# Performance work log

Measured on AMD Instinct MI355X. Metric: run time of the kernel, lower is better.

## Reference

```python
import jax, jax.numpy as jnp
import numpy as np

MASK_THRESHOLD = 0.5
NO_OVERLAP = True


def setup_inputs() -> dict:
    key = jax.random.key(0)
    B, N, C, M = 2, 50, 80, 28
    H, W = 800, 1333
    k1, k2, k3, k4, k5, k6, k7 = jax.random.split(key, 7)
    mask_outs = jax.random.uniform(k1, (B, N, C, M, M), dtype=jnp.float32)
    # valid xyxy boxes inside the image, 20-220 px per side
    cx = jax.random.uniform(k2, (B, N), dtype=jnp.float32) * W
    cy = jax.random.uniform(k3, (B, N), dtype=jnp.float32) * H
    bw = jax.random.uniform(k4, (B, N), dtype=jnp.float32) * 200.0 + 20.0
    bh = jax.random.uniform(k5, (B, N), dtype=jnp.float32) * 200.0 + 20.0
    boxes = jnp.stack([cx - bw / 2, cy - bh / 2, cx + bw / 2, cy + bh / 2], axis=-1)
    scores = jax.random.uniform(k6, (B, N), dtype=jnp.float32)
    class_ids = jax.random.randint(k7, (B, N), 0, C).astype(jnp.int64)
    return {"mask_outs": mask_outs, "boxes": boxes, "scores": scores,
            "class_ids": class_ids, "orig_h": H, "orig_w": W}


def _gather_rows(m, idx, size):
    # m: [Mh, Mw], idx: [L] int32 -> [L, Mw], zero outside [0, size)
    valid = (idx >= 0) & (idx < size)
    v = m[jnp.clip(idx, 0, size - 1)]
    return v * valid[:, None].astype(m.dtype)


def _gather_cols(m, idx, size):
    # m: [H, Mw], idx: [L] int32 -> [H, L], zero outside [0, size)
    valid = (idx >= 0) & (idx < size)
    v = m[:, jnp.clip(idx, 0, size - 1)]
    return v * valid[None, :].astype(m.dtype)


def _paste_soft(masks, boxes, H, W):
    # Equivalent to torch grid_sample(align_corners=False, zeros padding) on the
    # affine grid built from boxes (detectron2 _do_paste_mask), exploiting the
    # separable (outer-product) structure of the grid.
    # masks: [N, Mh, Mw], boxes: [N, 4] -> [N, H, W] float
    N, Mh, Mw = masks.shape
    x0, y0, x1, y1 = (boxes[:, 0:1], boxes[:, 1:2], boxes[:, 2:3], boxes[:, 3:4])
    img_y = jnp.arange(H, dtype=masks.dtype) + 0.5  # [H]
    img_x = jnp.arange(W, dtype=masks.dtype) + 0.5  # [W]
    gy = (img_y[None, :] - y0) / (y1 - y0) * 2.0 - 1.0  # [N, H] normalized
    gx = (img_x[None, :] - x0) / (x1 - x0) * 2.0 - 1.0  # [N, W]
    iy = ((gy + 1.0) * Mh - 1.0) / 2.0  # unnormalize, align_corners=False
    ix = ((gx + 1.0) * Mw - 1.0) / 2.0
    # --- bilinear along y: [N, Mh, Mw] -> [N, H, Mw]
    iy0 = jnp.floor(iy)
    wy = (iy - iy0)[..., None]
    iy0i = iy0.astype(jnp.int32)
    ry0 = jax.vmap(_gather_rows, in_axes=(0, 0, None))(masks, iy0i, Mh)
    ry1 = jax.vmap(_gather_rows, in_axes=(0, 0, None))(masks, iy0i + 1, Mh)
    rows = ry0 * (1.0 - wy) + ry1 * wy  # [N, H, Mw]
    # --- bilinear along x: [N, H, Mw] -> [N, H, W]
    ix0 = jnp.floor(ix)
    wx = (ix - ix0)[:, None, :]
    ix0i = ix0.astype(jnp.int32)
    cx0 = jax.vmap(_gather_cols, in_axes=(0, 0, None))(rows, ix0i, Mw)
    cx1 = jax.vmap(_gather_cols, in_axes=(0, 0, None))(rows, ix0i + 1, Mw)
    return cx0 * (1.0 - wx) + cx1 * wx  # [N, H, W]


def _remove_overlap(masks, scores):
    # Highest-scoring mask claims each pixel (matches sequential fg-suppression).
    order = jnp.argsort(-scores)
    sm = masks[order].astype(jnp.int32)  # [N, H, W]
    prev_cover = jnp.cumsum(sm, axis=0) - sm  # masks covering pixel before i
    keep = (sm > 0) & (prev_cover == 0)
    inv = jnp.argsort(order)
    return keep[inv]


def reference(mask_outs, boxes, scores, class_ids, orig_h, orig_w):
    # select class-specific mask: [B, N, C, M, M] -> [B, N, M, M]
    idx = class_ids.astype(jnp.int32)[:, :, None, None, None]
    sel = jnp.take_along_axis(mask_outs, idx, axis=2)[:, :, 0]
    soft = jax.vmap(lambda m, b: _paste_soft(m, b, orig_h, orig_w))(sel, boxes)
    masks = soft >= MASK_THRESHOLD  # [B, N, H, W] bool
    if NO_OVERLAP:
        masks = jax.vmap(_remove_overlap)(masks, scores)
    return masks, scores, class_ids
```

## Files before the change

### kernel.cpp

```cpp
#include <hip/hip_runtime.h>

#define NDET 50
#define BN   100
#define NC   80
#define MM   28
#define IMH  800
#define IMW  1333
#define HW   (IMH * IMW)

struct Params {
    float ylo, yhi, xlo, xhi;
    float y0, x0, dh, dw;
    float score;
    int   base;
};

__global__ void det2mask_setup(const float* __restrict__ boxes,
                               const float* __restrict__ scores,
                               const int*   __restrict__ class_ids,
                               Params* __restrict__ ps,
                               float* __restrict__ out_tail) {
#pragma clang fp contract(off)
    int i = threadIdx.x;
    if (i < BN) {
        float x0 = boxes[i * 4 + 0];
        float y0 = boxes[i * 4 + 1];
        float x1 = boxes[i * 4 + 2];
        float y1 = boxes[i * 4 + 3];
        float dw = x1 - x0;
        float dh = y1 - y0;
        Params p;
        p.y0 = y0; p.x0 = x0; p.dh = dh; p.dw = dw;
        p.ylo = y0 - dh * (0.5f / 28.0f) - 1.0f;
        p.yhi = y1 + dh * (0.5f / 28.0f) + 1.0f;
        p.xlo = x0 - dw * (0.5f / 28.0f) - 1.0f;
        p.xhi = x1 + dw * (0.5f / 28.0f) + 1.0f;
        p.score = scores[i];
        int cls = class_ids[i];
        p.base = (i * NC + cls) * (MM * MM);
        ps[i] = p;
        out_tail[i]      = scores[i];
        out_tail[BN + i] = (float)cls;
    }
}

__global__ __launch_bounds__(256) void det2mask_main(
        const float* __restrict__ mask_outs,
        const Params* __restrict__ ps,
        float* __restrict__ out) {
#pragma clang fp contract(off)
    __shared__ Params sp[NDET];
    const int b = blockIdx.z;
    {
        const int* src = (const int*)(ps + b * NDET);
        int* dst = (int*)sp;
        for (int i = threadIdx.x; i < NDET * 10; i += 256) dst[i] = src[i];
    }
    __syncthreads();

    const int x = blockIdx.x * 256 + threadIdx.x;
    const int y = blockIdx.y;
    const float px = (float)x + 0.5f;
    const float py = (float)y + 0.5f;

    int best = -1;
    float bs = -1.0f;

    for (int n = 0; n < NDET; ++n) {
        if (py <= sp[n].ylo || py >= sp[n].yhi) continue;
        if (px <= sp[n].xlo || px >= sp[n].xhi) continue;

        float gy = (py - sp[n].y0) / sp[n].dh * 2.0f - 1.0f;
        float iy = ((gy + 1.0f) * 28.0f - 1.0f) / 2.0f;
        float fy = floorf(iy);
        float wy = iy - fy;
        int iy0 = (int)fy;

        float gx = (px - sp[n].x0) / sp[n].dw * 2.0f - 1.0f;
        float ix = ((gx + 1.0f) * 28.0f - 1.0f) / 2.0f;
        float fx = floorf(ix);
        float wx = ix - fx;
        int ix0 = (int)fx;

        const float* mp = mask_outs + sp[n].base;
        int yc0 = min(max(iy0, 0), MM - 1);
        int yc1 = min(max(iy0 + 1, 0), MM - 1);
        int xc0 = min(max(ix0, 0), MM - 1);
        int xc1 = min(max(ix0 + 1, 0), MM - 1);
        bool r0 = (iy0 >= 0) && (iy0 <= MM - 1);
        bool r1 = (iy0 >= -1) && (iy0 <= MM - 2);
        bool c0 = (ix0 >= 0) && (ix0 <= MM - 1);
        bool c1 = (ix0 >= -1) && (ix0 <= MM - 2);

        float v00 = (r0 && c0) ? mp[yc0 * MM + xc0] : 0.0f;
        float v10 = (r1 && c0) ? mp[yc1 * MM + xc0] : 0.0f;
        float v01 = (r0 && c1) ? mp[yc0 * MM + xc1] : 0.0f;
        float v11 = (r1 && c1) ? mp[yc1 * MM + xc1] : 0.0f;

        float rr0 = v00 * (1.0f - wy) + v10 * wy;
        float rr1 = v01 * (1.0f - wy) + v11 * wy;
        float val = rr0 * (1.0f - wx) + rr1 * wx;

        if (val >= 0.5f && sp[n].score > bs) { bs = sp[n].score; best = n; }
    }

    if (x < IMW) {
        float* op = out + (size_t)b * NDET * HW + (size_t)y * IMW + x;
        for (int n = 0; n < NDET; ++n) {
            op[(size_t)n * HW] = (n == best) ? 1.0f : 0.0f;
        }
    }
}

extern "C" void kernel_launch(void* const* d_in, const int* in_sizes, int n_in,
                              void* d_out, int out_size, void* d_ws, size_t ws_size,
                              hipStream_t stream) {
    const float* mask_outs = (const float*)d_in[0];
    const float* boxes     = (const float*)d_in[1];
    const float* scores    = (const float*)d_in[2];
    const int*   class_ids = (const int*)d_in[3];
    float* out = (float*)d_out;
    Params* ps = (Params*)d_ws;

    hipLaunchKernelGGL(det2mask_setup, dim3(1), dim3(128), 0, stream,
                       boxes, scores, class_ids, ps, out + (size_t)BN * HW);

    dim3 grid((IMW + 255) / 256, IMH, 2);
    hipLaunchKernelGGL(det2mask_main, grid, dim3(256), 0, stream,
                       mask_outs, ps, out);
}
```

Measured before the change: 514.1 us.

## Vectorize mask output stores and precompute per-row box list in shared memory

Each block handles one image row. The first wavefront keeps only the detections whose vertical extent covers that row, compacts them with a ballot, and precomputes the row weights and row base offsets in shared memory. Each thread then handles four pixels and writes 16-byte float4 stores aligned to the row's phase, with a scalar path for the row edges. The aim is to cut store transactions on the output, which is dominated by writes, and to skip redundant per-box y work. In exchange the indexing is more complex, blocks are smaller (128 threads), and more work is done per thread.

```diff
diff --git a/kernel.cpp b/kernel.cpp
--- a/kernel.cpp
+++ b/kernel.cpp
@@ -44,70 +44,121 @@
     }
 }
 
-__global__ __launch_bounds__(256) void det2mask_main(
+__global__ __launch_bounds__(128) void det2mask_main(
         const float* __restrict__ mask_outs,
         const Params* __restrict__ ps,
         float* __restrict__ out) {
 #pragma clang fp contract(off)
-    __shared__ Params sp[NDET];
+    __shared__ float s_xlo[NDET], s_xhi[NDET], s_x0[NDET], s_dw[NDET];
+    __shared__ float s_sc[NDET], s_wy[NDET];
+    __shared__ int   s_rb0[NDET], s_rb1[NDET], s_n[NDET];
+    __shared__ int   s_ns;
+
     const int b = blockIdx.z;
-    {
-        const int* src = (const int*)(ps + b * NDET);
-        int* dst = (int*)sp;
-        for (int i = threadIdx.x; i < NDET * 10; i += 256) dst[i] = src[i];
+    const int y = blockIdx.y;
+    const float py = (float)y + 0.5f;
+    const int tid = threadIdx.x;
+
+    if (tid < 64) {
+        bool cov = false;
+        Params p;
+        if (tid < NDET) {
+            p = ps[b * NDET + tid];
+            cov = (py > p.ylo) && (py < p.yhi);
+        }
+        unsigned long long m = __ballot(cov);
+        if (cov) {
+            int pos = __popcll(m & ((1ull << tid) - 1ull));
+            float gy = (py - p.y0) / p.dh * 2.0f - 1.0f;
+            float iy = ((gy + 1.0f) * 28.0f - 1.0f) / 2.0f;
+            float fy = floorf(iy);
+            float wy = iy - fy;
+            int iy0 = (int)fy;
+            bool r0 = (iy0 >= 0) && (iy0 <= MM - 1);
+            bool r1 = (iy0 >= -1) && (iy0 <= MM - 2);
+            int yc0 = min(max(iy0, 0), MM - 1);
+            int yc1 = min(max(iy0 + 1, 0), MM - 1);
+            s_xlo[pos] = p.xlo; s_xhi[pos] = p.xhi;
+            s_x0[pos] = p.x0;   s_dw[pos] = p.dw;
+            s_sc[pos] = p.score; s_wy[pos] = wy;
+            s_rb0[pos] = r0 ? (p.base + yc0 * MM) : -1;
+            s_rb1[pos] = r1 ? (p.base + yc1 * MM) : -1;
+            s_n[pos] = tid;
+        }
+        if (tid == 0) s_ns = __popcll(m);
     }
     __syncthreads();
 
-    const int x = blockIdx.x * 256 + threadIdx.x;
-    const int y = blockIdx.y;
-    const float px = (float)x + 0.5f;
-    const float py = (float)y + 0.5f;
+    const int ns = s_ns;
+    const int sOff = (4 - (y & 3)) & 3;
+    const int nq = (IMW - sOff) >> 2;
+    const int t = blockIdx.x * 128 + tid;
 
-    int best = -1;
-    float bs = -1.0f;
+    int xs, cnt;
+    bool vec = false;
+    if (t < nq)            { xs = sOff + 4 * t;  cnt = 4;         vec = true; }
+    else if (t == nq)      { xs = sOff + 4 * nq; cnt = IMW - xs;  }
+    else if (t == nq + 1)  { xs = 0;             cnt = sOff;      }
+    else                   { xs = 0;             cnt = 0;         }
 
-    for (int n = 0; n < NDET; ++n) {
-        if (py <= sp[n].ylo || py >= sp[n].yhi) continue;
-        if (px <= sp[n].xlo || px >= sp[n].xhi) continue;
-
-        float gy = (py - sp[n].y0) / sp[n].dh * 2.0f - 1.0f;
-        float iy = ((gy + 1.0f) * 28.0f - 1.0f) / 2.0f;
-        float fy = floorf(iy);
-        float wy = iy - fy;
-        int iy0 = (int)fy;
-
-        float gx = (px - sp[n].x0) / sp[n].dw * 2.0f - 1.0f;
-        float ix = ((gx + 1.0f) * 28.0f - 1.0f) / 2.0f;
-        float fx = floorf(ix);
-        float wx = ix - fx;
-        int ix0 = (int)fx;
-
-        const float* mp = mask_outs + sp[n].base;
-        int yc0 = min(max(iy0, 0), MM - 1);
-        int yc1 = min(max(iy0 + 1, 0), MM - 1);
-        int xc0 = min(max(ix0, 0), MM - 1);
-        int xc1 = min(max(ix0 + 1, 0), MM - 1);
-        bool r0 = (iy0 >= 0) && (iy0 <= MM - 1);
-        bool r1 = (iy0 >= -1) && (iy0 <= MM - 2);
-        bool c0 = (ix0 >= 0) && (ix0 <= MM - 1);
-        bool c1 = (ix0 >= -1) && (ix0 <= MM - 2);
-
-        float v00 = (r0 && c0) ? mp[yc0 * MM + xc0] : 0.0f;
-        float v10 = (r1 && c0) ? mp[yc1 * MM + xc0] : 0.0f;
-        float v01 = (r0 && c1) ? mp[yc0 * MM + xc1] : 0.0f;
-        float v11 = (r1 && c1) ? mp[yc1 * MM + xc1] : 0.0f;
-
-        float rr0 = v00 * (1.0f - wy) + v10 * wy;
-        float rr1 = v01 * (1.0f - wy) + v11 * wy;
-        float val = rr0 * (1.0f - wx) + rr1 * wx;
-
-        if (val >= 0.5f && sp[n].score > bs) { bs = sp[n].score; best = n; }
+    int best[4] = {-1, -1, -1, -1};
+    if (cnt > 0) {
+        float bs[4] = {-1.0f, -1.0f, -1.0f, -1.0f};
+        const float qlo = (float)xs + 0.5f;
+        const float qhi = (float)(xs + cnt - 1) + 0.5f;
+        for (int s2 = 0; s2 < ns; ++s2) {
+            float xlo = s_xlo[s2], xhi = s_xhi[s2];
+            if (qhi <= xlo || qlo >= xhi) continue;
+            float x0 = s_x0[s2], dw = s_dw[s2];
+            float wy = s_wy[s2], sc = s_sc[s2];
+            int rb0 = s_rb0[s2], rb1 = s_rb1[s2];
+            int n = s_n[s2];
+#pragma unroll
+            for (int k = 0; k < 4; ++k) {
+                if (k >= cnt) break;
+                float px = (float)(xs + k) + 0.5f;
+                if (px <= xlo || px >= xhi) continue;
+                float gx = (px - x0) / dw * 2.0f - 1.0f;
+                float ix = ((gx + 1.0f) * 28.0f - 1.0f) / 2.0f;
+                float fx = floorf(ix);
+                float wx = ix - fx;
+                int ix0 = (int)fx;
+                bool c0 = (ix0 >= 0) && (ix0 <= MM - 1);
+                bool c1 = (ix0 >= -1) && (ix0 <= MM - 2);
+                int xc0 = min(max(ix0, 0), MM - 1);
+                int xc1 = min(max(ix0 + 1, 0), MM - 1);
+                float v00 = (rb0 >= 0 && c0) ? mask_outs[rb0 + xc0] : 0.0f;
+                float v10 = (rb1 >= 0 && c0) ? mask_outs[rb1 + xc0] : 0.0f;
+                float v01 = (rb0 >= 0 && c1) ? mask_outs[rb0 + xc1] : 0.0f;
+                float v11 = (rb1 >= 0 && c1) ? mask_outs[rb1 + xc1] : 0.0f;
+                float rr0 = v00 * (1.0f - wy) + v10 * wy;
+                float rr1 = v01 * (1.0f - wy) + v11 * wy;
+                float val = rr0 * (1.0f - wx) + rr1 * wx;
+                if (val >= 0.5f && sc > bs[k]) { bs[k] = sc; best[k] = n; }
+            }
+        }
     }
 
-    if (x < IMW) {
-        float* op = out + (size_t)b * NDET * HW + (size_t)y * IMW + x;
-        for (int n = 0; n < NDET; ++n) {
-            op[(size_t)n * HW] = (n == best) ? 1.0f : 0.0f;
+    if (cnt > 0) {
+        float* op = out + (size_t)b * NDET * HW + (size_t)y * IMW + xs;
+        if (vec) {
+            for (int n = 0; n < NDET; ++n) {
+                float4 v;
+                v.x = (best[0] == n) ? 1.0f : 0.0f;
+                v.y = (best[1] == n) ? 1.0f : 0.0f;
+                v.z = (best[2] == n) ? 1.0f : 0.0f;
+                v.w = (best[3] == n) ? 1.0f : 0.0f;
+                *reinterpret_cast<float4*>(op) = v;
+                op += HW;
+            }
+        } else {
+            for (int n = 0; n < NDET; ++n) {
+#pragma unroll
+                for (int k = 0; k < 3; ++k) {
+                    if (k < cnt) op[k] = (best[k] == n) ? 1.0f : 0.0f;
+                }
+                op += HW;
+            }
         }
     }
 }
@@ -125,7 +176,7 @@
     hipLaunchKernelGGL(det2mask_setup, dim3(1), dim3(128), 0, stream,
                        boxes, scores, class_ids, ps, out + (size_t)BN * HW);
 
-    dim3 grid((IMW + 255) / 256, IMH, 2);
-    hipLaunchKernelGGL(det2mask_main, grid, dim3(256), 0, stream,
+    dim3 grid(3, IMH, 2);
+    hipLaunchKernelGGL(det2mask_main, grid, dim3(128), 0, stream,
                        mask_outs, ps, out);
 }
```

After: 513.5 us. Within noise of the previous version (-0.1%).
